# Kernel tuning notes

Hardware: AMD Instinct MI355X
Metric: run time of the kernel (lower is better)

The kernel has to match this reference:

```python
import jax, jax.numpy as jnp
import numpy as np

ROPE_BASE = 10000.0

def apply_rope(x):
    # x: [B, S, H, Dh]  (rotate-half / NeoX convention)
    B, S, H, Dh = x.shape
    inv_freq = 1.0 / (ROPE_BASE ** (jnp.arange(0, Dh, 2, dtype=jnp.float32) / Dh))  # [Dh/2]
    ang = jnp.arange(S, dtype=jnp.float32)[:, None] * inv_freq[None, :]             # [S, Dh/2]
    cos = jnp.cos(ang)[None, :, None, :].astype(x.dtype)  # [1,S,1,Dh/2]
    sin = jnp.sin(ang)[None, :, None, :].astype(x.dtype)
    x1, x2 = jnp.split(x, 2, axis=-1)
    return jnp.concatenate([x1 * cos - x2 * sin, x1 * sin + x2 * cos], axis=-1)

def setup_inputs() -> dict:
    key = jax.random.key(0)
    k1, k2, k3 = jax.random.split(key, 3)
    B, S, D = 2, 2048, 1024
    x = jax.random.normal(k1, (B, S, D), dtype=jnp.float32)
    attn_mask = jnp.ones((B, S), dtype=bool)
    qkv_w = jax.random.normal(k2, (D, 3 * D), dtype=jnp.float32) * (1.0 / np.sqrt(D))
    out_w = jax.random.normal(k3, (D, D), dtype=jnp.float32) * (1.0 / np.sqrt(D))
    return {"x": x, "qkv_w": qkv_w, "out_w": out_w, "attn_mask": attn_mask, "is_causal": 1}

def reference(x, qkv_w, out_w, attn_mask, is_causal):
    B, S, D = x.shape
    H = 16
    Dh = D // H
    qkv = x @ qkv_w                                  # [B,S,3D]
    q, k, v = jnp.split(qkv, 3, axis=-1)
    q = apply_rope(q.reshape(B, S, H, Dh))           # [B,S,H,Dh]
    k = apply_rope(k.reshape(B, S, H, Dh))
    v = v.reshape(B, S, H, Dh)
    scale = 1.0 / np.sqrt(Dh)
    att = jnp.einsum('bqhd,bkhd->bhqk', q, k) * scale  # [B,H,S,S]
    if is_causal:
        mask = jnp.tril(jnp.ones((S, S), dtype=bool))[None, None]
    else:
        mask = attn_mask[:, None, None, :]             # [B,1,1,S]
    att = jnp.where(mask, att, jnp.finfo(att.dtype).min)
    p = jax.nn.softmax(att, axis=-1)
    y = jnp.einsum('bhqk,bkhd->bqhd', p, v).reshape(B, S, D)
    return y @ out_w
```

## Files before the change

### kernel.cpp

```cpp
#include <hip/hip_runtime.h>
#include <hip/hip_bf16.h>

#define BB 2
#define SS 2048
#define DD 1024
#define HH 16
#define N3 3072

#define POH (32 * 16 * 64 * 64)
#define PLH (32 * 16 * 64)

typedef __attribute__((ext_vector_type(8))) short bf16x8;
typedef __attribute__((ext_vector_type(4))) float f32x4;
typedef __attribute__((ext_vector_type(2))) unsigned int u32x2;

__device__ __forceinline__ float b2f(unsigned short u) {
    return __uint_as_float(((unsigned int)u) << 16);
}
__device__ __forceinline__ unsigned short f2b(float f) {
    unsigned int x = __float_as_uint(f);
    x += 0x7fffu + ((x >> 16) & 1u);
    return (unsigned short)(x >> 16);
}
__device__ __forceinline__ unsigned int pack2bf(float a, float b) {
    __hip_bfloat162 h = __float22bfloat162_rn(make_float2(a, b));
    return *(unsigned int*)&h;
}

__device__ __forceinline__ void gload_lds16(const void* g, void* l) {
    __builtin_amdgcn_global_load_lds(
        (__attribute__((address_space(1))) void*)g,
        (__attribute__((address_space(3))) void*)l, 16, 0, 0);
}

__global__ __launch_bounds__(256) void prep(
    const float* __restrict__ x,
    const float* __restrict__ qkv_w,
    const float* __restrict__ out_w,
    unsigned short* __restrict__ xb,
    unsigned short* __restrict__ w1t,
    unsigned short* __restrict__ w2t,
    float2* __restrict__ tab)
{
    __shared__ unsigned short tile[64][66];
    const int bid = blockIdx.x;
    const int tid = threadIdx.x;

    if (bid < 4096) {
        const int i = (bid * 256 + tid) * 4;
        float4 f = *(const float4*)(x + i);
        uint2 o;
        o.x = pack2bf(f.x, f.y);
        o.y = pack2bf(f.z, f.w);
        *(uint2*)(xb + i) = o;
        return;
    }

    const float* src;
    unsigned short* dst;
    int R, C, bx, by;
    if (bid < 4864) {
        const int t = bid - 4096;
        src = qkv_w; dst = w1t; R = DD; C = N3;
        bx = t % 48; by = t / 48;
    } else if (bid < 5120) {
        const int t = bid - 4864;
        src = out_w; dst = w2t; R = DD; C = DD;
        bx = t % 16; by = t / 16;
    } else {
        const int i = (bid - 5120) * 256 + tid;
        const int t = i & 31;
        const int s = i >> 5;
        float inv = powf(10000.0f, -(float)t * (1.0f / 32.0f));
        float sn, c;
        sincosf((float)s * inv, &sn, &c);
        tab[i] = make_float2(c, sn);
        return;
    }

    const int c0 = bx * 64, r0 = by * 64;
    const int lr = tid >> 4;
    const int lc = (tid & 15) * 4;
    #pragma unroll
    for (int i = 0; i < 4; ++i) {
        float4 f = *(const float4*)(src + (size_t)(r0 + lr + i * 16) * C + c0 + lc);
        tile[lr + i * 16][lc + 0] = f2b(f.x);
        tile[lr + i * 16][lc + 1] = f2b(f.y);
        tile[lr + i * 16][lc + 2] = f2b(f.z);
        tile[lr + i * 16][lc + 3] = f2b(f.w);
    }
    __syncthreads();
    #pragma unroll
    for (int i = 0; i < 4; ++i) {
        const int wr = lr + i * 16;
        ushort4 o;
        o.x = tile[lc + 0][wr];
        o.y = tile[lc + 1][wr];
        o.z = tile[lc + 2][wr];
        o.w = tile[lc + 3][wr];
        *(ushort4*)(dst + (size_t)(c0 + wr) * R + r0 + lc) = o;
    }
}

__global__ __launch_bounds__(256) void gemm_qkv_rope(
    const unsigned short* __restrict__ A,
    const unsigned short* __restrict__ Bt,
    const float2* __restrict__ tab,
    unsigned short* __restrict__ qo,
    unsigned short* __restrict__ ko,
    unsigned short* __restrict__ vt)
{
    constexpr int K = DD;
    constexpr int nbx = N3 / 128;
    __shared__ unsigned short Al[2][128 * 32];
    __shared__ unsigned short Bl[2][128 * 32];
    const int tid  = threadIdx.x;
    const int wave = tid >> 6;
    const int lane = tid & 63;
    const int quad = lane >> 4;
    const int l16  = lane & 15;

    const int per = gridDim.x >> 3;
    const int idx = (blockIdx.x & 7) * per + (blockIdx.x >> 3);
    const int m0 = (idx / nbx) * 128;
    const int n0 = (idx % nbx) * 128;
    const int wm = (wave >> 1) * 64;
    const int wn = (wave & 1) * 64;

    const int srow = wave * 32 + (lane >> 2);
    const int scol = (lane & 3) * 8;
    const unsigned short* gA = A  + (size_t)(m0 + srow) * K + scol;
    const unsigned short* gB = Bt + (size_t)(n0 + srow) * K + scol;

    f32x4 acc[4][4];
    #pragma unroll
    for (int mi = 0; mi < 4; ++mi)
        #pragma unroll
        for (int ni = 0; ni < 4; ++ni)
            acc[mi][ni] = (f32x4){0.f, 0.f, 0.f, 0.f};

    auto stage = [&](int k0, int buf) {
        #pragma unroll
        for (int i = 0; i < 2; ++i) {
            gload_lds16(gA + (size_t)i * 16 * K + k0, Al[buf] + (wave * 2 + i) * 512);
            gload_lds16(gB + (size_t)i * 16 * K + k0, Bl[buf] + (wave * 2 + i) * 512);
        }
    };

    stage(0, 0);
    int cur = 0;
    for (int k0 = 0; k0 < K; k0 += 32) {
        __syncthreads();
        if (k0 + 32 < K) stage(k0 + 32, cur ^ 1);

        bf16x8 af[4], bfr[4];
        #pragma unroll
        for (int mi = 0; mi < 4; ++mi)
            af[mi] = *(const bf16x8*)&Al[cur][(wm + mi * 16 + l16) * 32 + quad * 8];
        #pragma unroll
        for (int ni = 0; ni < 4; ++ni)
            bfr[ni] = *(const bf16x8*)&Bl[cur][(wn + ni * 16 + l16) * 32 + quad * 8];
        #pragma unroll
        for (int mi = 0; mi < 4; ++mi)
            #pragma unroll
            for (int ni = 0; ni < 4; ++ni)
                acc[mi][ni] = __builtin_amdgcn_mfma_f32_16x16x32_bf16(
                    af[mi], bfr[ni], acc[mi][ni], 0, 0, 0);
        cur ^= 1;
    }

    const int gc  = n0 + wn;
    const int sec = gc >> 10;
    const int h   = (gc & 1023) >> 6;
    const int s0g = m0 + wm;
    const int b   = s0g >> 11;
    const size_t bh = (size_t)b * HH + h;

    if (sec < 2) {
        const float SCq = (sec == 0) ? 0.18033688011112042f : 1.0f;
        unsigned short* dst = (sec == 0) ? qo : ko;
        #pragma unroll
        for (int mi = 0; mi < 4; ++mi) {
            #pragma unroll
            for (int r = 0; r < 4; ++r) {
                const int ss = (s0g + mi * 16 + quad * 4 + r) & (SS - 1);
                const float2* tp = tab + (size_t)ss * 32;
                unsigned short* row = dst + (bh * SS + ss) * 64;
                #pragma unroll
                for (int ni = 0; ni < 2; ++ni) {
                    const int t = ni * 16 + l16;
                    float2 cs = tp[t];
                    const float x1 = acc[mi][ni][r];
                    const float x2 = acc[mi][ni + 2][r];
                    row[t]      = f2b((x1 * cs.x - x2 * cs.y) * SCq);
                    row[t + 32] = f2b((x1 * cs.y + x2 * cs.x) * SCq);
                }
            }
        }
    } else {
        #pragma unroll
        for (int mi = 0; mi < 4; ++mi) {
            const int ss0 = (s0g + mi * 16 + quad * 4) & (SS - 1);
            #pragma unroll
            for (int ni = 0; ni < 4; ++ni) {
                const int d = ni * 16 + l16;
                ushort4 o;
                o.x = f2b(acc[mi][ni][0]);
                o.y = f2b(acc[mi][ni][1]);
                o.z = f2b(acc[mi][ni][2]);
                o.w = f2b(acc[mi][ni][3]);
                *(ushort4*)(vt + (bh * 64 + d) * SS + ss0) = o;
            }
        }
    }
}

__global__ __launch_bounds__(256) void gemm_out(
    const unsigned short* __restrict__ A,
    const unsigned short* __restrict__ Bt,
    float* __restrict__ C)
{
    constexpr int K = DD;
    constexpr int nbx = DD / 64;
    __shared__ unsigned short Al[2][64 * 32];
    __shared__ unsigned short Bl[2][64 * 32];
    const int tid  = threadIdx.x;
    const int wave = tid >> 6;
    const int lane = tid & 63;
    const int quad = lane >> 4;
    const int l16  = lane & 15;

    const int per = gridDim.x >> 3;
    const int idx = (blockIdx.x & 7) * per + (blockIdx.x >> 3);
    const int m0 = (idx / nbx) * 64;
    const int n0 = (idx % nbx) * 64;
    const int wm = (wave >> 1) * 32;
    const int wn = (wave & 1) * 32;

    const int srow = wave * 16 + (lane >> 2);
    const int scol = (lane & 3) * 8;
    const unsigned short* gA = A  + (size_t)(m0 + srow) * K + scol;
    const unsigned short* gB = Bt + (size_t)(n0 + srow) * K + scol;

    f32x4 acc[2][2];
    #pragma unroll
    for (int mi = 0; mi < 2; ++mi)
        #pragma unroll
        for (int ni = 0; ni < 2; ++ni)
            acc[mi][ni] = (f32x4){0.f, 0.f, 0.f, 0.f};

    auto stage = [&](int k0, int buf) {
        gload_lds16(gA + k0, Al[buf] + wave * 512);
        gload_lds16(gB + k0, Bl[buf] + wave * 512);
    };

    stage(0, 0);
    int cur = 0;
    for (int k0 = 0; k0 < K; k0 += 32) {
        __syncthreads();
        if (k0 + 32 < K) stage(k0 + 32, cur ^ 1);

        bf16x8 af[2], bfr[2];
        #pragma unroll
        for (int mi = 0; mi < 2; ++mi)
            af[mi] = *(const bf16x8*)&Al[cur][(wm + mi * 16 + l16) * 32 + quad * 8];
        #pragma unroll
        for (int ni = 0; ni < 2; ++ni)
            bfr[ni] = *(const bf16x8*)&Bl[cur][(wn + ni * 16 + l16) * 32 + quad * 8];
        #pragma unroll
        for (int mi = 0; mi < 2; ++mi)
            #pragma unroll
            for (int ni = 0; ni < 2; ++ni)
                acc[mi][ni] = __builtin_amdgcn_mfma_f32_16x16x32_bf16(
                    af[mi], bfr[ni], acc[mi][ni], 0, 0, 0);
        cur ^= 1;
    }

    #pragma unroll
    for (int mi = 0; mi < 2; ++mi) {
        #pragma unroll
        for (int r = 0; r < 4; ++r) {
            const size_t base = (size_t)(m0 + wm + mi * 16 + quad * 4 + r) * DD + n0 + wn;
            #pragma unroll
            for (int ni = 0; ni < 2; ++ni)
                C[base + ni * 16 + l16] = acc[mi][ni][r];
        }
    }
}

__device__ __forceinline__ void attn_step(
    const unsigned short* __restrict__ Kb,
    const unsigned short* __restrict__ Vb,
    const bf16x8 qf0, const bf16x8 qf1, const bf16x8 onesf,
    f32x4 O[4], f32x4& l_acc,
    bool diag, const unsigned char* mrow,
    int kt, int quad, int l16, int csw, int qg)
{
    f32x4 Sf[4];
    __builtin_amdgcn_s_setprio(1);
    #pragma unroll
    for (int st = 0; st < 4; ++st) {
        const unsigned short* kr = &Kb[(st * 16 + l16) * 64];
        bf16x8 kf0 = *(const bf16x8*)(kr + csw * 8);
        bf16x8 kf1 = *(const bf16x8*)(kr + (csw ^ 4) * 8);
        f32x4 s = (f32x4){0.f, 0.f, 0.f, 0.f};
        s = __builtin_amdgcn_mfma_f32_16x16x32_bf16(kf0, qf0, s, 0, 0, 0);
        s = __builtin_amdgcn_mfma_f32_16x16x32_bf16(kf1, qf1, s, 0, 0, 0);
        Sf[st] = s;
    }
    __builtin_amdgcn_s_setprio(0);

    if (diag) {
        #pragma unroll
        for (int st = 0; st < 4; ++st) {
            const int kb0 = kt * 64 + st * 16 + quad * 4;
            #pragma unroll
            for (int r = 0; r < 4; ++r)
                if (kb0 + r > qg) Sf[st][r] = -1e30f;
        }
    } else if (mrow) {
        #pragma unroll
        for (int st = 0; st < 4; ++st) {
            uchar4 mv = *(const uchar4*)(mrow + st * 16 + quad * 4);
            if (!mv.x) Sf[st][0] = -1e30f;
            if (!mv.y) Sf[st][1] = -1e30f;
            if (!mv.z) Sf[st][2] = -1e30f;
            if (!mv.w) Sf[st][3] = -1e30f;
        }
    }

    #pragma unroll
    for (int st = 0; st < 4; ++st)
        #pragma unroll
        for (int r = 0; r < 4; ++r)
            Sf[st][r] = exp2f(Sf[st][r]);

    unsigned int W[4][2];
    #pragma unroll
    for (int st = 0; st < 4; ++st) {
        W[st][0] = pack2bf(Sf[st][0], Sf[st][1]);
        W[st][1] = pack2bf(Sf[st][2], Sf[st][3]);
    }

    unsigned int pw0[4], pw1[4];
    #pragma unroll
    for (int j = 0; j < 2; ++j) {
        u32x2 s1 = __builtin_amdgcn_permlane32_swap(W[0][j], W[1][j], false, false);
        u32x2 s2 = __builtin_amdgcn_permlane16_swap(s1.x, s1.y, false, false);
        pw0[j]     = s2.x;
        pw0[j + 2] = s2.y;
        u32x2 t1 = __builtin_amdgcn_permlane32_swap(W[2][j], W[3][j], false, false);
        u32x2 t2 = __builtin_amdgcn_permlane16_swap(t1.x, t1.y, false, false);
        pw1[j]     = t2.x;
        pw1[j + 2] = t2.y;
    }
    bf16x8 pf0 = *(const bf16x8*)pw0;
    bf16x8 pf1 = *(const bf16x8*)pw1;

    __builtin_amdgcn_s_setprio(1);
    l_acc = __builtin_amdgcn_mfma_f32_16x16x32_bf16(onesf, pf0, l_acc, 0, 0, 0);
    l_acc = __builtin_amdgcn_mfma_f32_16x16x32_bf16(onesf, pf1, l_acc, 0, 0, 0);
    #pragma unroll
    for (int st = 0; st < 4; ++st) {
        const unsigned short* vr = &Vb[(st * 16 + l16) * 64];
        bf16x8 vf0 = *(const bf16x8*)(vr + csw * 8);
        bf16x8 vf1 = *(const bf16x8*)(vr + (csw ^ 4) * 8);
        O[st] = __builtin_amdgcn_mfma_f32_16x16x32_bf16(vf0, pf0, O[st], 0, 0, 0);
        O[st] = __builtin_amdgcn_mfma_f32_16x16x32_bf16(vf1, pf1, O[st], 0, 0, 0);
    }
    __builtin_amdgcn_s_setprio(0);
}

__global__ __launch_bounds__(256) void flash_attn(
    const unsigned short* __restrict__ q,
    const unsigned short* __restrict__ k,
    const unsigned short* __restrict__ vt,
    unsigned short* __restrict__ y,
    float* __restrict__ pO,
    float* __restrict__ pL,
    const int* __restrict__ is_causal,
    const unsigned char* __restrict__ attn_mask)
{
    __shared__ unsigned short Kl[2][64 * 64];
    __shared__ unsigned short Vl[2][64 * 64];

    const int bid  = blockIdx.x;
    const int work = (bid & 7) * 192 + (bid >> 3);
    const int bhi  = work / 48;
    const int s    = work % 48;
    const int b = bhi >> 4;
    const int h = bhi & 15;
    const bool causal = (is_causal[0] != 0);

    int tile, k0t, k1t;
    bool split;
    if (s < 16) {
        tile = 16 + s; k0t = 0; k1t = 15; split = true;
    } else {
        const int r = s - 16, p = r >> 1;
        if (r & 1) { tile = 15 - p; k0t = 0;  k1t = causal ? tile : 31; split = false; }
        else       { tile = 31 - p; k0t = 16; k1t = causal ? tile : 31; split = true;  }
    }
    const int half = (s < 16) ? 0 : 1;

    const int tid  = threadIdx.x;
    const int wave = tid >> 6;
    const int lane = tid & 63;
    const int quad = lane >> 4;
    const int l16  = lane & 15;

    const size_t bh = (size_t)b * HH + h;

    const int qg = tile * 64 + wave * 16 + l16;
    const unsigned short* qrow = q + (bh * SS + qg) * 64;
    const bf16x8 qf0 = *(const bf16x8*)(qrow + quad * 8);
    const bf16x8 qf1 = *(const bf16x8*)(qrow + 32 + quad * 8);

    bf16x8 onesf;
    #pragma unroll
    for (int i = 0; i < 8; ++i) onesf[i] = (short)0x3F80;

    const unsigned short* kbase  = k  + bh * SS * 64;
    const unsigned short* vtbase = vt + bh * 64 * SS;

    const int Rl  = lane >> 3;
    const int cph = lane & 7;
    const int csw = quad ^ (l16 & 7);

    f32x4 O[4];
    #pragma unroll
    for (int st = 0; st < 4; ++st) O[st] = (f32x4){0.f, 0.f, 0.f, 0.f};
    f32x4 l_acc = (f32x4){0.f, 0.f, 0.f, 0.f};

    auto stage = [&](int kt) {
        const int buf = kt & 1;
        #pragma unroll
        for (int i = 0; i < 2; ++i) {
            const int jj = wave * 2 + i;
            const int R  = jj * 8 + Rl;
            const int cl = cph ^ (R & 7);
            gload_lds16(kbase + ((size_t)(kt * 64 + R) * 64 + cl * 8),
                        &Kl[buf][jj * 512]);
            gload_lds16(vtbase + ((size_t)R * SS + kt * 64 + cl * 8),
                        &Vl[buf][jj * 512]);
        }
    };

    stage(k0t);
    for (int kt = k0t; kt <= k1t; ++kt) {
        __syncthreads();
        if (kt + 1 <= k1t) stage(kt + 1);

        const unsigned char* mrow = causal ? nullptr
                                           : (attn_mask + (size_t)b * SS + kt * 64);
        attn_step(Kl[kt & 1], Vl[kt & 1], qf0, qf1, onesf, O, l_acc,
                  causal && kt == tile, mrow, kt, quad, l16, csw, qg);
    }

    if (!split) {
        const float inv = 1.0f / l_acc[0];
        unsigned short* yrow = y + ((size_t)b * SS + qg) * DD + h * 64;
        #pragma unroll
        for (int st = 0; st < 4; ++st) {
            uint2 o;
            o.x = pack2bf(O[st][0] * inv, O[st][1] * inv);
            o.y = pack2bf(O[st][2] * inv, O[st][3] * inv);
            *(uint2*)(yrow + st * 16 + quad * 4) = o;
        }
    } else {
        float* ob = pO + (size_t)half * POH
                  + (((bh * 16 + (size_t)(tile - 16)) * 64 + wave * 16 + l16) * 64);
        #pragma unroll
        for (int st = 0; st < 4; ++st)
            *(f32x4*)(ob + st * 16 + quad * 4) = O[st];
        if (quad == 0)
            pL[(size_t)half * PLH + (bh * 16 + (size_t)(tile - 16)) * 64
               + wave * 16 + l16] = l_acc[0];
    }
}

__global__ __launch_bounds__(256) void attn_merge(
    const float* __restrict__ pO, const float* __restrict__ pL,
    unsigned short* __restrict__ y)
{
    const int i = (blockIdx.x * 256 + threadIdx.x) * 4;
    float4 oa = *(const float4*)(pO + i);
    float4 obv = *(const float4*)(pO + POH + i);
    const int rowi = i >> 6;
    const int d    = i & 63;
    const float inv = 1.0f / (pL[rowi] + pL[PLH + rowi]);
    const int row = rowi & 63;
    const int tt  = (rowi >> 6) & 15;
    const int bh  = rowi >> 10;
    const int b = bh >> 4, h = bh & 15;
    const int sq = (16 + tt) * 64 + row;
    unsigned short* yp = y + ((size_t)b * SS + sq) * DD + h * 64 + d;
    uint2 ov;
    ov.x = pack2bf((oa.x + obv.x) * inv, (oa.y + obv.y) * inv);
    ov.y = pack2bf((oa.z + obv.z) * inv, (oa.w + obv.w) * inv);
    *(uint2*)yp = ov;
}

extern "C" void kernel_launch(void* const* d_in, const int* in_sizes, int n_in,
                              void* d_out, int out_size, void* d_ws, size_t ws_size,
                              hipStream_t stream) {
    const float* x      = (const float*)d_in[0];
    const float* qkv_w  = (const float*)d_in[1];
    const float* out_w  = (const float*)d_in[2];
    const unsigned char* mask = (const unsigned char*)d_in[3];
    const int*   is_c   = (const int*)d_in[4];
    float* out = (float*)d_out;

    unsigned short* xb  = (unsigned short*)d_ws;
    unsigned short* w1t = xb  + (size_t)4096 * 1024;
    unsigned short* w2t = w1t + (size_t)3072 * 1024;
    unsigned short* qkv = w2t + (size_t)1024 * 1024;
    unsigned short* qb  = qkv + (size_t)4096 * 3072;
    unsigned short* kb  = qb  + (size_t)BB * HH * SS * 64;
    unsigned short* vt  = kb  + (size_t)BB * HH * SS * 64;
    float2* tab = (float2*)(vt + (size_t)BB * HH * SS * 64);
    unsigned short* yb = xb;

    float* pO = (float*)qkv;
    float* pL = pO + (size_t)2 * POH;

    prep<<<5376, 256, 0, stream>>>(x, qkv_w, out_w, xb, w1t, w2t, tab);

    gemm_qkv_rope<<<(N3 / 128) * (4096 / 128), 256, 0, stream>>>(
        xb, w1t, tab, qb, kb, vt);

    flash_attn<<<dim3(48 * BB * HH), 256, 0, stream>>>(qb, kb, vt, yb, pO, pL,
                                                       is_c, mask);

    attn_merge<<<2048, 256, 0, stream>>>(pO, pL, yb);

    gemm_out<<<1024, 256, 0, stream>>>(yb, w2t, out);
}
```

Before: 193.7 us.

## Split causal attention KV range into three-way chunks for better load balance

Changes the flash attention work decomposition from a two-way split of the upper query tiles to 12-tile KV chunks. Tiles 12-23 are split in two and tiles 24-31 in three, giving 60 work items per batch-head with a smaller maximum per block. The merge kernel now sums two or three partial outputs and denominators per row. This adds more partial writes and merge traffic in exchange for shorter critical-path blocks, and pL storage is relocated into the rope table region.

```diff
diff --git a/kernel.cpp b/kernel.cpp
--- a/kernel.cpp
+++ b/kernel.cpp
@@ -7,8 +7,7 @@
 #define HH 16
 #define N3 3072
 
-#define POH (32 * 16 * 64 * 64)
-#define PLH (32 * 16 * 64)
+#define NINST 48
 
 typedef __attribute__((ext_vector_type(8))) short bf16x8;
 typedef __attribute__((ext_vector_type(4))) float f32x4;
@@ -385,23 +384,25 @@
     __shared__ unsigned short Vl[2][64 * 64];
 
     const int bid  = blockIdx.x;
-    const int work = (bid & 7) * 192 + (bid >> 3);
-    const int bhi  = work / 48;
-    const int s    = work % 48;
+    const int work = (bid & 7) * 240 + (bid >> 3);
+    const int bhi  = work / 60;
+    const int s    = work % 60;
     const int b = bhi >> 4;
     const int h = bhi & 15;
     const bool causal = (is_causal[0] != 0);
 
-    int tile, k0t, k1t;
-    bool split;
-    if (s < 16) {
-        tile = 16 + s; k0t = 0; k1t = 15; split = true;
-    } else {
-        const int r = s - 16, p = r >> 1;
-        if (r & 1) { tile = 15 - p; k0t = 0;  k1t = causal ? tile : 31; split = false; }
-        else       { tile = 31 - p; k0t = 16; k1t = causal ? tile : 31; split = true;  }
-    }
-    const int half = (s < 16) ? 0 : 1;
+    int tile, c;
+    if (s < 20)      { tile = 12 + s;        c = 0;  }
+    else if (s < 28) { tile = 24 + (s - 20); c = 1;  }
+    else if (s < 40) { tile = 11 - (s - 28); c = -1; }
+    else if (s < 52) { tile = 23 - (s - 40); c = 1;  }
+    else             { tile = 31 - (s - 52); c = 2;  }
+    const bool split = (c >= 0);
+    const int lastc  = (tile <= 11) ? 0 : (tile <= 23 ? 1 : 2);
+    const int k0t = split ? c * 12 : 0;
+    const int k1t = causal
+        ? (split ? min(tile, c * 12 + 11) : tile)
+        : ((!split || c == lastc) ? 31 : c * 12 + 11);
 
     const int tid  = threadIdx.x;
     const int wave = tid >> 6;
@@ -468,14 +469,14 @@
             *(uint2*)(yrow + st * 16 + quad * 4) = o;
         }
     } else {
-        float* ob = pO + (size_t)half * POH
-                  + (((bh * 16 + (size_t)(tile - 16)) * 64 + wave * 16 + l16) * 64);
+        const int inst = (tile <= 23) ? (tile - 12) * 2 + c
+                                      : 24 + (tile - 24) * 3 + c;
+        float* ob = pO + ((bh * NINST + (size_t)inst) * 64 + wave * 16 + l16) * 64;
         #pragma unroll
         for (int st = 0; st < 4; ++st)
             *(f32x4*)(ob + st * 16 + quad * 4) = O[st];
         if (quad == 0)
-            pL[(size_t)half * PLH + (bh * 16 + (size_t)(tile - 16)) * 64
-               + wave * 16 + l16] = l_acc[0];
+            pL[(bh * NINST + (size_t)inst) * 64 + wave * 16 + l16] = l_acc[0];
     }
 }
 
@@ -484,20 +485,31 @@
     unsigned short* __restrict__ y)
 {
     const int i = (blockIdx.x * 256 + threadIdx.x) * 4;
-    float4 oa = *(const float4*)(pO + i);
-    float4 obv = *(const float4*)(pO + POH + i);
+    const int d    = i & 63;
     const int rowi = i >> 6;
-    const int d    = i & 63;
-    const float inv = 1.0f / (pL[rowi] + pL[PLH + rowi]);
-    const int row = rowi & 63;
-    const int tt  = (rowi >> 6) & 15;
-    const int bh  = rowi >> 10;
+    const int row  = rowi & 63;
+    const int rg   = rowi >> 6;
+    const int tt   = rg % 20;
+    const int bh   = rg / 20;
+    const int tile = 12 + tt;
+    const int ib   = (tt < 12) ? tt * 2 : 24 + (tt - 12) * 3;
+    const int nc   = (tt < 12) ? 2 : 3;
+
+    float4 o = make_float4(0.f, 0.f, 0.f, 0.f);
+    float l = 0.f;
+    for (int cc = 0; cc < nc; ++cc) {
+        const size_t base = ((size_t)bh * NINST + ib + cc);
+        float4 oc = *(const float4*)(pO + (base * 64 + row) * 64 + d);
+        o.x += oc.x; o.y += oc.y; o.z += oc.z; o.w += oc.w;
+        l += pL[base * 64 + row];
+    }
+    const float inv = 1.0f / l;
     const int b = bh >> 4, h = bh & 15;
-    const int sq = (16 + tt) * 64 + row;
+    const int sq = tile * 64 + row;
     unsigned short* yp = y + ((size_t)b * SS + sq) * DD + h * 64 + d;
     uint2 ov;
-    ov.x = pack2bf((oa.x + obv.x) * inv, (oa.y + obv.y) * inv);
-    ov.y = pack2bf((oa.z + obv.z) * inv, (oa.w + obv.w) * inv);
+    ov.x = pack2bf(o.x * inv, o.y * inv);
+    ov.y = pack2bf(o.z * inv, o.w * inv);
     *(uint2*)yp = ov;
 }
 
@@ -522,17 +534,17 @@
     unsigned short* yb = xb;
 
     float* pO = (float*)qkv;
-    float* pL = pO + (size_t)2 * POH;
+    float* pL = (float*)tab;
 
     prep<<<5376, 256, 0, stream>>>(x, qkv_w, out_w, xb, w1t, w2t, tab);
 
     gemm_qkv_rope<<<(N3 / 128) * (4096 / 128), 256, 0, stream>>>(
         xb, w1t, tab, qb, kb, vt);
 
-    flash_attn<<<dim3(48 * BB * HH), 256, 0, stream>>>(qb, kb, vt, yb, pO, pL,
-                                                       is_c, mask);
-
-    attn_merge<<<2048, 256, 0, stream>>>(pO, pL, yb);
+    flash_attn<<<dim3(1920), 256, 0, stream>>>(qb, kb, vt, yb, pO, pL,
+                                               is_c, mask);
+
+    attn_merge<<<2560, 256, 0, stream>>>(pO, pL, yb);
 
     gemm_out<<<1024, 256, 0, stream>>>(yb, w2t, out);
 }
```

Result: slower. 198.6 us (+2.5%).

## Process two 16-row query subtiles per wave in flash attention with 128 threads

Applied to the files above, without the earlier changes.

Flash attention blocks drop from four waves to two. Each wave now handles 32 query rows as two 16-row subtiles, so every K and V fragment read from LDS feeds twice as many MFMAs. Each thread also issues twice as many global-to-LDS loads per tile. The trade-off is more accumulator registers and fewer waves per block to hide latency, in exchange for halving LDS fragment reads per unit of compute.

```diff
diff --git a/kernel.cpp b/kernel.cpp
--- a/kernel.cpp
+++ b/kernel.cpp
@@ -288,28 +288,10 @@
     }
 }
 
-__device__ __forceinline__ void attn_step(
-    const unsigned short* __restrict__ Kb,
-    const unsigned short* __restrict__ Vb,
-    const bf16x8 qf0, const bf16x8 qf1, const bf16x8 onesf,
-    f32x4 O[4], f32x4& l_acc,
-    bool diag, const unsigned char* mrow,
-    int kt, int quad, int l16, int csw, int qg)
+__device__ __forceinline__ void softmax_perm(
+    f32x4 Sf[4], bool diag, const unsigned char* mrow, int kt, int qg,
+    int quad, bf16x8& pf0, bf16x8& pf1)
 {
-    f32x4 Sf[4];
-    __builtin_amdgcn_s_setprio(1);
-    #pragma unroll
-    for (int st = 0; st < 4; ++st) {
-        const unsigned short* kr = &Kb[(st * 16 + l16) * 64];
-        bf16x8 kf0 = *(const bf16x8*)(kr + csw * 8);
-        bf16x8 kf1 = *(const bf16x8*)(kr + (csw ^ 4) * 8);
-        f32x4 s = (f32x4){0.f, 0.f, 0.f, 0.f};
-        s = __builtin_amdgcn_mfma_f32_16x16x32_bf16(kf0, qf0, s, 0, 0, 0);
-        s = __builtin_amdgcn_mfma_f32_16x16x32_bf16(kf1, qf1, s, 0, 0, 0);
-        Sf[st] = s;
-    }
-    __builtin_amdgcn_s_setprio(0);
-
     if (diag) {
         #pragma unroll
         for (int st = 0; st < 4; ++st) {
@@ -354,24 +336,11 @@
         pw1[j]     = t2.x;
         pw1[j + 2] = t2.y;
     }
-    bf16x8 pf0 = *(const bf16x8*)pw0;
-    bf16x8 pf1 = *(const bf16x8*)pw1;
-
-    __builtin_amdgcn_s_setprio(1);
-    l_acc = __builtin_amdgcn_mfma_f32_16x16x32_bf16(onesf, pf0, l_acc, 0, 0, 0);
-    l_acc = __builtin_amdgcn_mfma_f32_16x16x32_bf16(onesf, pf1, l_acc, 0, 0, 0);
-    #pragma unroll
-    for (int st = 0; st < 4; ++st) {
-        const unsigned short* vr = &Vb[(st * 16 + l16) * 64];
-        bf16x8 vf0 = *(const bf16x8*)(vr + csw * 8);
-        bf16x8 vf1 = *(const bf16x8*)(vr + (csw ^ 4) * 8);
-        O[st] = __builtin_amdgcn_mfma_f32_16x16x32_bf16(vf0, pf0, O[st], 0, 0, 0);
-        O[st] = __builtin_amdgcn_mfma_f32_16x16x32_bf16(vf1, pf1, O[st], 0, 0, 0);
-    }
-    __builtin_amdgcn_s_setprio(0);
-}
-
-__global__ __launch_bounds__(256) void flash_attn(
+    pf0 = *(const bf16x8*)pw0;
+    pf1 = *(const bf16x8*)pw1;
+}
+
+__global__ __launch_bounds__(128) void flash_attn(
     const unsigned short* __restrict__ q,
     const unsigned short* __restrict__ k,
     const unsigned short* __restrict__ vt,
@@ -411,10 +380,14 @@
 
     const size_t bh = (size_t)b * HH + h;
 
-    const int qg = tile * 64 + wave * 16 + l16;
-    const unsigned short* qrow = q + (bh * SS + qg) * 64;
-    const bf16x8 qf0 = *(const bf16x8*)(qrow + quad * 8);
-    const bf16x8 qf1 = *(const bf16x8*)(qrow + 32 + quad * 8);
+    const int qgA = tile * 64 + wave * 32 + l16;
+    const int qgB = qgA + 16;
+    const unsigned short* qrowA = q + (bh * SS + qgA) * 64;
+    const unsigned short* qrowB = q + (bh * SS + qgB) * 64;
+    const bf16x8 qfA0 = *(const bf16x8*)(qrowA + quad * 8);
+    const bf16x8 qfA1 = *(const bf16x8*)(qrowA + 32 + quad * 8);
+    const bf16x8 qfB0 = *(const bf16x8*)(qrowB + quad * 8);
+    const bf16x8 qfB1 = *(const bf16x8*)(qrowB + 32 + quad * 8);
 
     bf16x8 onesf;
     #pragma unroll
@@ -427,16 +400,20 @@
     const int cph = lane & 7;
     const int csw = quad ^ (l16 & 7);
 
-    f32x4 O[4];
-    #pragma unroll
-    for (int st = 0; st < 4; ++st) O[st] = (f32x4){0.f, 0.f, 0.f, 0.f};
-    f32x4 l_acc = (f32x4){0.f, 0.f, 0.f, 0.f};
+    f32x4 OA[4], OB[4];
+    #pragma unroll
+    for (int st = 0; st < 4; ++st) {
+        OA[st] = (f32x4){0.f, 0.f, 0.f, 0.f};
+        OB[st] = (f32x4){0.f, 0.f, 0.f, 0.f};
+    }
+    f32x4 lA = (f32x4){0.f, 0.f, 0.f, 0.f};
+    f32x4 lB = (f32x4){0.f, 0.f, 0.f, 0.f};
 
     auto stage = [&](int kt) {
         const int buf = kt & 1;
         #pragma unroll
-        for (int i = 0; i < 2; ++i) {
-            const int jj = wave * 2 + i;
+        for (int i = 0; i < 4; ++i) {
+            const int jj = wave * 4 + i;
             const int R  = jj * 8 + Rl;
             const int cl = cph ^ (R & 7);
             gload_lds16(kbase + ((size_t)(kt * 64 + R) * 64 + cl * 8),
@@ -451,31 +428,87 @@
         __syncthreads();
         if (kt + 1 <= k1t) stage(kt + 1);
 
+        const unsigned short* Kb = Kl[kt & 1];
+        const unsigned short* Vb = Vl[kt & 1];
+        const bool diag = causal && (kt == tile);
         const unsigned char* mrow = causal ? nullptr
                                            : (attn_mask + (size_t)b * SS + kt * 64);
-        attn_step(Kl[kt & 1], Vl[kt & 1], qf0, qf1, onesf, O, l_acc,
-                  causal && kt == tile, mrow, kt, quad, l16, csw, qg);
+
+        f32x4 SA[4], SB[4];
+        __builtin_amdgcn_s_setprio(1);
+        #pragma unroll
+        for (int st = 0; st < 4; ++st) {
+            const unsigned short* kr = &Kb[(st * 16 + l16) * 64];
+            bf16x8 kf0 = *(const bf16x8*)(kr + csw * 8);
+            bf16x8 kf1 = *(const bf16x8*)(kr + (csw ^ 4) * 8);
+            f32x4 sa = (f32x4){0.f, 0.f, 0.f, 0.f};
+            sa = __builtin_amdgcn_mfma_f32_16x16x32_bf16(kf0, qfA0, sa, 0, 0, 0);
+            sa = __builtin_amdgcn_mfma_f32_16x16x32_bf16(kf1, qfA1, sa, 0, 0, 0);
+            SA[st] = sa;
+            f32x4 sb = (f32x4){0.f, 0.f, 0.f, 0.f};
+            sb = __builtin_amdgcn_mfma_f32_16x16x32_bf16(kf0, qfB0, sb, 0, 0, 0);
+            sb = __builtin_amdgcn_mfma_f32_16x16x32_bf16(kf1, qfB1, sb, 0, 0, 0);
+            SB[st] = sb;
+        }
+        __builtin_amdgcn_s_setprio(0);
+
+        bf16x8 pfA0, pfA1, pfB0, pfB1;
+        softmax_perm(SA, diag, mrow, kt, qgA, quad, pfA0, pfA1);
+        softmax_perm(SB, diag, mrow, kt, qgB, quad, pfB0, pfB1);
+
+        __builtin_amdgcn_s_setprio(1);
+        lA = __builtin_amdgcn_mfma_f32_16x16x32_bf16(onesf, pfA0, lA, 0, 0, 0);
+        lA = __builtin_amdgcn_mfma_f32_16x16x32_bf16(onesf, pfA1, lA, 0, 0, 0);
+        lB = __builtin_amdgcn_mfma_f32_16x16x32_bf16(onesf, pfB0, lB, 0, 0, 0);
+        lB = __builtin_amdgcn_mfma_f32_16x16x32_bf16(onesf, pfB1, lB, 0, 0, 0);
+        #pragma unroll
+        for (int st = 0; st < 4; ++st) {
+            const unsigned short* vr = &Vb[(st * 16 + l16) * 64];
+            bf16x8 vf0 = *(const bf16x8*)(vr + csw * 8);
+            bf16x8 vf1 = *(const bf16x8*)(vr + (csw ^ 4) * 8);
+            OA[st] = __builtin_amdgcn_mfma_f32_16x16x32_bf16(vf0, pfA0, OA[st], 0, 0, 0);
+            OA[st] = __builtin_amdgcn_mfma_f32_16x16x32_bf16(vf1, pfA1, OA[st], 0, 0, 0);
+            OB[st] = __builtin_amdgcn_mfma_f32_16x16x32_bf16(vf0, pfB0, OB[st], 0, 0, 0);
+            OB[st] = __builtin_amdgcn_mfma_f32_16x16x32_bf16(vf1, pfB1, OB[st], 0, 0, 0);
+        }
+        __builtin_amdgcn_s_setprio(0);
     }
 
     if (!split) {
-        const float inv = 1.0f / l_acc[0];
-        unsigned short* yrow = y + ((size_t)b * SS + qg) * DD + h * 64;
+        const float invA = 1.0f / lA[0];
+        unsigned short* yrowA = y + ((size_t)b * SS + qgA) * DD + h * 64;
         #pragma unroll
         for (int st = 0; st < 4; ++st) {
             uint2 o;
-            o.x = pack2bf(O[st][0] * inv, O[st][1] * inv);
-            o.y = pack2bf(O[st][2] * inv, O[st][3] * inv);
-            *(uint2*)(yrow + st * 16 + quad * 4) = o;
+            o.x = pack2bf(OA[st][0] * invA, OA[st][1] * invA);
+            o.y = pack2bf(OA[st][2] * invA, OA[st][3] * invA);
+            *(uint2*)(yrowA + st * 16 + quad * 4) = o;
+        }
+        const float invB = 1.0f / lB[0];
+        unsigned short* yrowB = y + ((size_t)b * SS + qgB) * DD + h * 64;
+        #pragma unroll
+        for (int st = 0; st < 4; ++st) {
+            uint2 o;
+            o.x = pack2bf(OB[st][0] * invB, OB[st][1] * invB);
+            o.y = pack2bf(OB[st][2] * invB, OB[st][3] * invB);
+            *(uint2*)(yrowB + st * 16 + quad * 4) = o;
         }
     } else {
-        float* ob = pO + (size_t)half * POH
-                  + (((bh * 16 + (size_t)(tile - 16)) * 64 + wave * 16 + l16) * 64);
-        #pragma unroll
-        for (int st = 0; st < 4; ++st)
-            *(f32x4*)(ob + st * 16 + quad * 4) = O[st];
-        if (quad == 0)
-            pL[(size_t)half * PLH + (bh * 16 + (size_t)(tile - 16)) * 64
-               + wave * 16 + l16] = l_acc[0];
+        const size_t tbase = (size_t)half * POH
+                           + ((bh * 16 + (size_t)(tile - 16)) * 64) * 64;
+        float* obA = pO + tbase + (size_t)(wave * 32 + l16) * 64;
+        float* obB = obA + 16 * 64;
+        #pragma unroll
+        for (int st = 0; st < 4; ++st) {
+            *(f32x4*)(obA + st * 16 + quad * 4) = OA[st];
+            *(f32x4*)(obB + st * 16 + quad * 4) = OB[st];
+        }
+        if (quad == 0) {
+            const size_t lbase = (size_t)half * PLH
+                               + (bh * 16 + (size_t)(tile - 16)) * 64;
+            pL[lbase + wave * 32 + l16]      = lA[0];
+            pL[lbase + wave * 32 + 16 + l16] = lB[0];
+        }
     }
 }
 
@@ -529,7 +562,7 @@
     gemm_qkv_rope<<<(N3 / 128) * (4096 / 128), 256, 0, stream>>>(
         xb, w1t, tab, qb, kb, vt);
 
-    flash_attn<<<dim3(48 * BB * HH), 256, 0, stream>>>(qb, kb, vt, yb, pO, pL,
+    flash_attn<<<dim3(48 * BB * HH), 128, 0, stream>>>(qb, kb, vt, yb, pO, pL,
                                                        is_c, mask);
 
     attn_merge<<<2048, 256, 0, stream>>>(pO, pL, yb);
```

Result: slower. 204.6 us (+5.6%).
